# Performance work log

Measured on AMD Instinct MI355X. Metric: run time of the kernel, lower is better.

## Reference

```python
import math
import jax, jax.numpy as jnp
import numpy as np

NUM_HEADS = 8
NUM_LANDMARKS = 64
MP_ITERS = 6


def moore_penrose_iter_pinv(x, iters=MP_ITERS):
    # x: [..., m, m]; iterative Newton-Schulz-style pseudo-inverse
    abs_x = jnp.abs(x)
    col = abs_x.sum(axis=-1)
    row = abs_x.sum(axis=-2)
    z = jnp.swapaxes(x, -1, -2) / (jnp.max(col) * jnp.max(row))
    I = jnp.eye(x.shape[-1], dtype=x.dtype)
    for _ in range(iters):
        xz = x @ z
        z = 0.25 * z @ (13.0 * I - xz @ (15.0 * I - xz @ (7.0 * I - xz)))
    return z


def setup_inputs() -> dict:
    key = jax.random.key(0)
    k_x, k_qkv, k_proj = jax.random.split(key, 3)
    B, T, E = 2, 2048, 512
    x = jax.random.normal(k_x, (B, T, E), dtype=jnp.float32)
    w_qkv = jax.random.normal(k_qkv, (E, 3 * E), dtype=jnp.float32) * 0.02
    b_qkv = jnp.zeros((3 * E,), dtype=jnp.float32)
    w_proj = jax.random.normal(k_proj, (E, E), dtype=jnp.float32) * 0.02
    b_proj = jnp.zeros((E,), dtype=jnp.float32)
    return {"x": x, "w_qkv": w_qkv, "b_qkv": b_qkv, "w_proj": w_proj, "b_proj": b_proj}


def reference(x, w_qkv, b_qkv, w_proj, b_proj):
    B, T, E = x.shape
    H = NUM_HEADS
    M = NUM_LANDMARKS
    hd = E // H
    # T chosen as a multiple of M so the original pad branch is a no-op
    qkv = x @ w_qkv + b_qkv  # [B,T,3E]
    q, k, v = jnp.split(qkv, 3, axis=-1)

    def to_heads(t):
        return t.reshape(B, T, H, hd).transpose(0, 2, 1, 3)  # [B,H,T,hd]

    q = to_heads(q) * (1.0 / math.sqrt(hd))
    k = to_heads(k)
    v = to_heads(v)

    l = T // M  # landmark group size
    q_landmarks = q.reshape(B, H, M, l, hd).mean(axis=3)  # [B,H,M,hd]
    k_landmarks = k.reshape(B, H, M, l, hd).mean(axis=3)  # [B,H,M,hd]

    q_kl = jnp.einsum('bhid,bhjd->bhij', q, k_landmarks)           # [B,H,T,M]
    ql_kl = jnp.einsum('bhid,bhjd->bhij', q_landmarks, k_landmarks)  # [B,H,M,M]
    ql_k = jnp.einsum('bhid,bhjd->bhij', q_landmarks, k)           # [B,H,M,T]

    neg_inf = float('-inf')
    mask_q_kl = jnp.tril(jnp.ones((T, M), dtype=bool))
    mask_ql_kl = jnp.tril(jnp.ones((M, M), dtype=bool))
    mask_ql_k = jnp.tril(jnp.ones((M, T), dtype=bool))

    F_t = jax.nn.softmax(jnp.where(mask_q_kl, q_kl, neg_inf), axis=-1)    # [B,H,T,M]
    A = jax.nn.softmax(jnp.where(mask_ql_kl, ql_kl, neg_inf), axis=-1)    # [B,H,M,M]
    B_t = jax.nn.softmax(jnp.where(mask_ql_k, ql_k, neg_inf), axis=-1)    # [B,H,M,T]

    A_t = moore_penrose_iter_pinv(A, iters=MP_ITERS)

    attn = (F_t @ A_t) @ B_t  # [B,H,T,T] (original materializes this for dropout)
    y = attn @ v              # [B,H,T,hd]
    y = y.transpose(0, 2, 1, 3).reshape(B, T, E)
    return y @ w_proj + b_proj
```

## Files before the change

kernel.cpp:

```cpp
#include <hip/hip_runtime.h>
#include <hip/hip_bf16.h>

#define TB 2048
#define EB 512

using short8 = __attribute__((ext_vector_type(8))) short;
using f32x4  = __attribute__((ext_vector_type(4))) float;

__global__ __launch_bounds__(256) void k_pool(const float* __restrict__ x,
                                              float* __restrict__ xp,
                                              unsigned int* __restrict__ scal_u) {
  if (blockIdx.x == 0 && threadIdx.x == 0) scal_u[0] = 0u;
  int idx = blockIdx.x * 256 + threadIdx.x;
  int b = idx >> 15;
  int rem = idx & 32767;
  int m = rem >> 9;
  int e = rem & 511;
  const float* src = x + (b * TB + m * 32) * EB + e;
  float s = 0.f;
#pragma unroll
  for (int i = 0; i < 32; ++i) s += src[i * EB];
  xp[idx] = s * (1.f / 32.f);
}

__device__ __forceinline__ int swz_idx(int row, int col) {
  return row * 64 + ((((col >> 3) ^ (row & 7)) << 3) | (col & 7));
}

__device__ __forceinline__ void split_bf(float v, ushort& h, ushort& l) {
  __hip_bfloat16 bh = __float2bfloat16(v);
  float fh = __bfloat162float(bh);
  __hip_bfloat16 bl = __float2bfloat16(v - fh);
  h = *(ushort*)&bh;
  l = *(ushort*)&bl;
}

__device__ __forceinline__ void mm_frags(const short8 ah[2], const short8 al[2],
                                         const ushort* bhp, const ushort* blp,
                                         int lane, f32x4 acc[4]) {
  const int g = lane >> 4, li = lane & 15;
#pragma unroll
  for (int nt = 0; nt < 4; ++nt) {
    f32x4 a = acc[nt];
#pragma unroll
    for (int kh = 0; kh < 2; ++kh) {
      int n = nt * 16 + li;
      int k0 = kh * 32 + 8 * g;
      int idx = n * 64 + ((((k0 >> 3) ^ (n & 7)) << 3));
      short8 bh = *(const short8*)&bhp[idx];
      short8 bl = *(const short8*)&blp[idx];
      a = __builtin_amdgcn_mfma_f32_16x16x32_bf16(al[kh], bh, a, 0, 0, 0);
      a = __builtin_amdgcn_mfma_f32_16x16x32_bf16(ah[kh], bl, a, 0, 0, 0);
      a = __builtin_amdgcn_mfma_f32_16x16x32_bf16(ah[kh], bh, a, 0, 0, 0);
    }
    acc[nt] = a;
  }
}

__device__ __forceinline__ void zero_acc(f32x4 acc[4]) {
#pragma unroll
  for (int nt = 0; nt < 4; ++nt) acc[nt] = (f32x4){0.f, 0.f, 0.f, 0.f};
}

__device__ __forceinline__ void softmax_rows(f32x4 s[4], int band, int g, int li,
                                             bool causal, int t0) {
#pragma unroll
  for (int r = 0; r < 4; ++r) {
    int trow = t0 + band + 4 * g + r;
    float m = -1e30f;
    float sv[4];
#pragma unroll
    for (int nt = 0; nt < 4; ++nt) {
      int col = nt * 16 + li;
      bool ok = !causal || (col <= trow);
      sv[nt] = ok ? s[nt][r] : -1e30f;
      m = fmaxf(m, sv[nt]);
    }
    m = fmaxf(m, __shfl_xor(m, 1));
    m = fmaxf(m, __shfl_xor(m, 2));
    m = fmaxf(m, __shfl_xor(m, 4));
    m = fmaxf(m, __shfl_xor(m, 8));
    float su = 0.f;
    float ee[4];
#pragma unroll
    for (int nt = 0; nt < 4; ++nt) {
      ee[nt] = (sv[nt] > -1e29f) ? __expf(sv[nt] - m) : 0.f;
      su += ee[nt];
    }
    su += __shfl_xor(su, 1);
    su += __shfl_xor(su, 2);
    su += __shfl_xor(su, 4);
    su += __shfl_xor(su, 8);
    float inv = 1.f / su;
#pragma unroll
    for (int nt = 0; nt < 4; ++nt) s[nt][r] = ee[nt] * inv;
  }
}

__device__ __forceinline__ void wrP(ushort* hp, ushort* lp, int lane,
                                    const f32x4 acc[4]) {
  const int g = lane >> 4, li = lane & 15;
#pragma unroll
  for (int nt = 0; nt < 4; ++nt) {
    int c = nt * 16 + li;
#pragma unroll
    for (int r = 0; r < 4; ++r) {
      int row = 4 * g + r;
      ushort h, l;
      split_bf(acc[nt][r], h, l);
      int idx = swz_idx(row, c);
      hp[idx] = h;
      lp[idx] = l;
    }
  }
}

__device__ __forceinline__ void ld_pfrags(const ushort* hp, const ushort* lp,
                                          int lane, short8 ah[2], short8 al[2]) {
  const int g = lane >> 4, li = lane & 15;
#pragma unroll
  for (int kh = 0; kh < 2; ++kh) {
    int k0 = kh * 32 + 8 * g;
    int idx = li * 64 + ((((k0 >> 3) ^ (li & 7)) << 3));
    ah[kh] = *(const short8*)&hp[idx];
    al[kh] = *(const short8*)&lp[idx];
  }
}

template <int MODE>
__global__ __launch_bounds__(256) void k_gemm_mfma(const float* __restrict__ A,
                                                   const float* __restrict__ A2,
                                                   const float* __restrict__ W,
                                                   const float* __restrict__ bias,
                                                   float* __restrict__ o0,
                                                   float* __restrict__ o1,
                                                   float* __restrict__ o2,
                                                   float* __restrict__ o3) {
  constexpr int LDW = (MODE == 1) ? 512 : 1536;
  __shared__ ushort Ah[4096], Al[4096], Bh[4096], Bl[4096];
  const int tid = threadIdx.x;
  const int lane = tid & 63, w = tid >> 6, band = w * 16;
  int bx, by;
  if constexpr (MODE == 0 || MODE == 1) {
    int bid = blockIdx.x;
    by = ((bid & 7) << 3) | (bid >> 6);
    bx = (bid >> 3) & 7;
  } else {
    bx = blockIdx.x;
    by = blockIdx.y;
  }
  const int variant = (MODE == 2) ? (by >> 1) : 0;
  const int m0 = (MODE == 2) ? ((by & 1) * 64) : by * 64;
  const int bcol0 = (MODE == 2) ? (variant == 0 ? 512 + bx * 64 : bx * 64)
                                : bx * 64;
  const int g = lane >> 4, li = lane & 15;

  const int arow = tid >> 2, akc = (tid & 3) * 16;
  const int bn = tid & 63, bkc = (tid >> 6) * 16;

  const float* asrc;
  {
    int gr = m0 + arow;
    if constexpr (MODE == 2) {
      asrc = (variant == 0) ? (A + ((gr >> 6) * TB + (gr & 63)) * EB)
                            : (A2 + gr * EB);
    } else {
      asrc = A + gr * EB;
    }
  }

  f32x4 acc[4];
  zero_acc(acc);

  float av[16], bv[16];
#pragma unroll
  for (int j = 0; j < 4; ++j)
    *(float4*)&av[j * 4] = *(const float4*)&asrc[akc + j * 4];
#pragma unroll
  for (int i = 0; i < 16; ++i) bv[i] = W[(bkc + i) * LDW + bcol0 + bn];

#pragma unroll
  for (int k0 = 0; k0 < 512; k0 += 64) {
    if (k0) __syncthreads();
#pragma unroll
    for (int c2 = 0; c2 < 2; ++c2) {
      short8 hv, lv;
#pragma unroll
      for (int i = 0; i < 8; ++i) {
        ushort h, l;
        split_bf(av[c2 * 8 + i], h, l);
        hv[i] = (short)h;
        lv[i] = (short)l;
      }
      int chunk = ((akc >> 3) + c2) ^ (arow & 7);
      int idx = arow * 64 + chunk * 8;
      *(short8*)&Ah[idx] = hv;
      *(short8*)&Al[idx] = lv;
    }
#pragma unroll
    for (int c2 = 0; c2 < 2; ++c2) {
      short8 hv, lv;
#pragma unroll
      for (int i = 0; i < 8; ++i) {
        ushort h, l;
        split_bf(bv[c2 * 8 + i], h, l);
        hv[i] = (short)h;
        lv[i] = (short)l;
      }
      int chunk = ((bkc >> 3) + c2) ^ (bn & 7);
      int idx = bn * 64 + chunk * 8;
      *(short8*)&Bh[idx] = hv;
      *(short8*)&Bl[idx] = lv;
    }
    __syncthreads();
    if (k0 + 64 < 512) {
#pragma unroll
      for (int j = 0; j < 4; ++j)
        *(float4*)&av[j * 4] = *(const float4*)&asrc[k0 + 64 + akc + j * 4];
#pragma unroll
      for (int i = 0; i < 16; ++i)
        bv[i] = W[(k0 + 64 + bkc + i) * LDW + bcol0 + bn];
    }
    short8 a_h[2], a_l[2];
    const int row = band + li;
#pragma unroll
    for (int kh = 0; kh < 2; ++kh) {
      int chunk = ((kh * 32 + 8 * g) >> 3) ^ (row & 7);
      int idx = row * 64 + chunk * 8;
      a_h[kh] = *(const short8*)&Ah[idx];
      a_l[kh] = *(const short8*)&Al[idx];
    }
    mm_frags(a_h, a_l, Bh, Bl, lane, acc);
  }
#pragma unroll
  for (int nt = 0; nt < 4; ++nt) {
#pragma unroll
    for (int r = 0; r < 4; ++r) {
      int trow = band + 4 * g + r;
      int gcol = bcol0 + nt * 16 + li;
      float v = acc[nt][r] + bias[gcol];
      if constexpr (MODE == 1) {
        o0[(m0 + trow) * 512 + gcol] = v;
      } else {
        int gr = m0 + trow;
        int b = gr >> 6, t = gr & 63;
        int cloc = (variant == 0) ? (gcol - 512) : gcol;
        int which = cloc >> 9;
        int hd_ = cloc & 511;
        int h = hd_ >> 6, d = hd_ & 63;
        int dst = ((b * 8 + h) * 64 + t) * 64 + d;
        if (variant == 0) {
          if (which == 0) o0[dst] = v; else o1[dst] = v;
        } else {
          if (which == 0) o2[dst] = v * 0.125f; else o3[dst] = v;
        }
      }
    }
  }
}

__global__ __launch_bounds__(256) void k_abv_w2(
    const float* __restrict__ qlg, const float* __restrict__ klg,
    const float* __restrict__ k64, const float* __restrict__ v64,
    const float* __restrict__ w_qkv, const float* __restrict__ b_qkv,
    float* __restrict__ A, float* __restrict__ BV,
    float* __restrict__ W2g, float* __restrict__ bcst,
    unsigned int* __restrict__ scal_u) {
  __shared__ ushort KLh[4096], KLl[4096], Kh[4096], Kl_[4096], VTh[4096], VTl[4096];
  __shared__ ushort Ph[4][1024], Pl[4][1024];
  __shared__ float red[4][64];
  const int tid = threadIdx.x;
  const int lane = tid & 63, w = tid >> 6, band = w * 16;
  const int g = lane >> 4, li = lane & 15;

  if (blockIdx.x >= 16) {
    const int bh = blockIdx.x - 16;
    const int h = bh & 7;
    const int base = bh * 4096;
    {
      int n = tid & 63, kc = (tid >> 6) * 16;
      float a[16];
#pragma unroll
      for (int i = 0; i < 16; ++i) a[i] = klg[base + n * 64 + kc + i];
#pragma unroll
      for (int c2 = 0; c2 < 2; ++c2) {
        int idx = n * 64 + ((((kc >> 3) + c2) ^ (n & 7)) << 3);
        short8 hv, lv;
#pragma unroll
        for (int i = 0; i < 8; ++i) {
          ushort hh, ll;
          split_bf(a[c2 * 8 + i], hh, ll);
          hv[i] = (short)hh;
          lv[i] = (short)ll;
        }
        *(short8*)&KLh[idx] = hv;
        *(short8*)&KLl[idx] = lv;
      }
    }
    __syncthreads();
    if (tid < 64) {
      float bc = 0.f;
      for (int d = 0; d < 64; ++d)
        bc += b_qkv[h * 64 + d] * klg[base + tid * 64 + d];
      bcst[bh * 64 + tid] = 0.125f * bc;
    }
#pragma unroll
    for (int m0 = 0; m0 < 512; m0 += 64) {
      short8 a_h[2], a_l[2];
      int row = m0 + band + li;
#pragma unroll
      for (int kh = 0; kh < 2; ++kh) {
        int d0 = kh * 32 + 8 * g;
        float tmp[8];
        *(float4*)&tmp[0] = *(const float4*)&w_qkv[row * 1536 + h * 64 + d0];
        *(float4*)&tmp[4] = *(const float4*)&w_qkv[row * 1536 + h * 64 + d0 + 4];
        short8 hv, lv;
#pragma unroll
        for (int i = 0; i < 8; ++i) {
          ushort hh, ll;
          split_bf(tmp[i], hh, ll);
          hv[i] = (short)hh;
          lv[i] = (short)ll;
        }
        a_h[kh] = hv;
        a_l[kh] = lv;
      }
      f32x4 acc[4];
      zero_acc(acc);
      mm_frags(a_h, a_l, KLh, KLl, lane, acc);
#pragma unroll
      for (int nt = 0; nt < 4; ++nt)
#pragma unroll
        for (int r = 0; r < 4; ++r)
          W2g[bh * 32768 + (m0 + band + 4 * g + r) * 64 + nt * 16 + li] =
              0.125f * acc[nt][r];
    }
    return;
  }

  const int bh = blockIdx.x;
  const int base = bh * 4096;
  {
    int n = tid & 63, kc = (tid >> 6) * 16;
    float a[16], b[16], c[16];
#pragma unroll
    for (int i = 0; i < 16; ++i) {
      a[i] = klg[base + n * 64 + kc + i];
      b[i] = k64[base + n * 64 + kc + i];
      c[i] = v64[base + (kc + i) * 64 + n];
    }
#pragma unroll
    for (int c2 = 0; c2 < 2; ++c2) {
      int idx = n * 64 + ((((kc >> 3) + c2) ^ (n & 7)) << 3);
      short8 hv, lv;
#pragma unroll
      for (int i = 0; i < 8; ++i) { ushort h, l; split_bf(a[c2*8+i], h, l); hv[i]=(short)h; lv[i]=(short)l; }
      *(short8*)&KLh[idx] = hv; *(short8*)&KLl[idx] = lv;
#pragma unroll
      for (int i = 0; i < 8; ++i) { ushort h, l; split_bf(b[c2*8+i], h, l); hv[i]=(short)h; lv[i]=(short)l; }
      *(short8*)&Kh[idx] = hv; *(short8*)&Kl_[idx] = lv;
#pragma unroll
      for (int i = 0; i < 8; ++i) { ushort h, l; split_bf(c[c2*8+i], h, l); hv[i]=(short)h; lv[i]=(short)l; }
      *(short8*)&VTh[idx] = hv; *(short8*)&VTl[idx] = lv;
    }
  }
  short8 q_h[2], q_l[2];
  {
    int row = band + li;
#pragma unroll
    for (int kh = 0; kh < 2; ++kh) {
      int k0 = kh * 32 + 8 * g;
      float tmp[8];
      *(float4*)&tmp[0] = *(const float4*)&qlg[base + row * 64 + k0];
      *(float4*)&tmp[4] = *(const float4*)&qlg[base + row * 64 + k0 + 4];
      short8 hv, lv;
#pragma unroll
      for (int i = 0; i < 8; ++i) { ushort h, l; split_bf(tmp[i], h, l); hv[i]=(short)h; lv[i]=(short)l; }
      q_h[kh] = hv; q_l[kh] = lv;
    }
  }
  __syncthreads();
  f32x4 s1[4];
  zero_acc(s1);
  mm_frags(q_h, q_l, KLh, KLl, lane, s1);
  softmax_rows(s1, band, g, li, true, 0);
#pragma unroll
  for (int nt = 0; nt < 4; ++nt)
#pragma unroll
    for (int r = 0; r < 4; ++r)
      A[base + (band + 4 * g + r) * 64 + nt * 16 + li] = s1[nt][r];
  {
    float part[4];
#pragma unroll
    for (int nt = 0; nt < 4; ++nt) {
      part[nt] = s1[nt][0] + s1[nt][1] + s1[nt][2] + s1[nt][3];
      part[nt] += __shfl_xor(part[nt], 16);
      part[nt] += __shfl_xor(part[nt], 32);
    }
    if (g == 0) {
#pragma unroll
      for (int nt = 0; nt < 4; ++nt) red[w][nt * 16 + li] = part[nt];
    }
    __syncthreads();
    if (tid < 64) {
      float t = red[0][tid] + red[1][tid] + red[2][tid] + red[3][tid];
#pragma unroll
      for (int off = 32; off; off >>= 1) t = fmaxf(t, __shfl_xor(t, off));
      if (tid == 0) atomicMax(scal_u, __float_as_uint(t));
    }
  }
  f32x4 s2[4];
  zero_acc(s2);
  mm_frags(q_h, q_l, Kh, Kl_, lane, s2);
  softmax_rows(s2, band, g, li, true, 0);
  wrP(Ph[w], Pl[w], lane, s2);
  short8 p_h[2], p_l[2];
  ld_pfrags(Ph[w], Pl[w], lane, p_h, p_l);
  f32x4 y[4];
  zero_acc(y);
  mm_frags(p_h, p_l, VTh, VTl, lane, y);
#pragma unroll
  for (int nt = 0; nt < 4; ++nt)
#pragma unroll
    for (int r = 0; r < 4; ++r)
      BV[base + (band + 4 * g + r) * 64 + nt * 16 + li] = y[nt][r];
}

__device__ __forceinline__ void ld_afrags(const ushort* hp, const ushort* lp,
                                          int band, int lane,
                                          short8 ah[2], short8 al[2]) {
  const int g = lane >> 4, li = lane & 15;
  const int row = band + li;
#pragma unroll
  for (int kh = 0; kh < 2; ++kh) {
    int k0 = kh * 32 + 8 * g;
    int idx = row * 64 + ((((k0 >> 3) ^ (row & 7)) << 3));
    ah[kh] = *(const short8*)&hp[idx];
    al[kh] = *(const short8*)&lp[idx];
  }
}

__device__ __forceinline__ void mm_frags0(const short8 ah[2], const short8 al[2],
                                          const ushort* bhp, const ushort* blp,
                                          int lane, f32x4 acc[4]) {
  zero_acc(acc);
  mm_frags(ah, al, bhp, blp, lane, acc);
}

__device__ __forceinline__ void wrT(ushort* hp, ushort* lp, int band, int lane,
                                    const f32x4 acc[4], float cI, float mul) {
  const int g = lane >> 4, li = lane & 15;
  const int r0 = band + 4 * g;
#pragma unroll
  for (int nt = 0; nt < 4; ++nt) {
    int c = nt * 16 + li;
    ushort h[4], l[4];
#pragma unroll
    for (int r = 0; r < 4; ++r) {
      float v = mul * acc[nt][r] + ((r0 + r) == c ? cI : 0.f);
      split_bf(v, h[r], l[r]);
    }
    int idx = c * 64 + (((((r0) >> 3) ^ (c & 7)) << 3) | (r0 & 7));
    *(ushort4*)&hp[idx] = make_ushort4(h[0], h[1], h[2], h[3]);
    *(ushort4*)&lp[idx] = make_ushort4(l[0], l[1], l[2], l[3]);
  }
}

__device__ __forceinline__ void wrN(ushort* hp, ushort* lp, int band, int lane,
                                    const f32x4 acc[4], float mul) {
  const int g = lane >> 4, li = lane & 15;
#pragma unroll
  for (int nt = 0; nt < 4; ++nt) {
    int c = nt * 16 + li;
#pragma unroll
    for (int r = 0; r < 4; ++r) {
      int row = band + 4 * g + r;
      ushort h, l;
      split_bf(mul * acc[nt][r], h, l);
      int idx = swz_idx(row, c);
      hp[idx] = h;
      lp[idx] = l;
    }
  }
}

__global__ __launch_bounds__(256) void k_pinv(const float* __restrict__ A,
                                              const float* __restrict__ BVg,
                                              const unsigned int* __restrict__ scal_u,
                                              float* __restrict__ C) {
  __shared__ ushort ZT_h[4096], ZT_l[4096], ZA_h[4096], ZA_l[4096],
                    PA_h[4096], PA_l[4096], QA_h[4096], QA_l[4096],
                    QB_h[4096], QB_l[4096], BT_h[4096], BT_l[4096];
  const int bh = blockIdx.x, tid = threadIdx.x;
  const int lane = tid & 63, w = tid >> 6, band = w * 16;
  const int base = bh * 4096;
  const float sc = 1.f / __uint_as_float(scal_u[0]);
  const float* Ag = A + base;
  const float* Bg = BVg + base;

  {
    int prow = tid >> 2;
    int pc0 = (tid & 3) * 16;
#pragma unroll 4
    for (int j = 0; j < 16; ++j) {
      int col = pc0 + j;
      float av = Ag[prow * 64 + col] * sc;
      ushort h, l;
      split_bf(av, h, l);
      int i1 = swz_idx(prow, col);
      ZT_h[i1] = h; ZT_l[i1] = l;
      int i2 = swz_idx(col, prow);
      ZA_h[i2] = h; ZA_l[i2] = l;
      float bv = Bg[prow * 64 + col];
      split_bf(bv, h, l);
      BT_h[i2] = h; BT_l[i2] = l;
    }
  }
  short8 a_h[2], a_l[2];
  {
    const int g = lane >> 4, li = lane & 15;
    int row = band + li;
#pragma unroll
    for (int kh = 0; kh < 2; ++kh) {
      int k0 = kh * 32 + 8 * g;
      float tmp[8];
      *(float4*)&tmp[0] = *(const float4*)&Ag[row * 64 + k0];
      *(float4*)&tmp[4] = *(const float4*)&Ag[row * 64 + k0 + 4];
      short8 hv, lv;
#pragma unroll
      for (int i = 0; i < 8; ++i) {
        ushort h, l;
        split_bf(tmp[i], h, l);
        hv[i] = (short)h;
        lv[i] = (short)l;
      }
      a_h[kh] = hv;
      a_l[kh] = lv;
    }
  }
  __syncthreads();

  for (int it = 0; it < 6; ++it) {
    f32x4 acc[4];
    mm_frags0(a_h, a_l, ZT_h, ZT_l, lane, acc);
    wrN(PA_h, PA_l, band, lane, acc, 1.f);
    wrT(QA_h, QA_l, band, lane, acc, 7.f, -1.f);
    __syncthreads();
    short8 p_h[2], p_l[2];
    ld_afrags(PA_h, PA_l, band, lane, p_h, p_l);
    mm_frags0(p_h, p_l, QA_h, QA_l, lane, acc);
    wrT(QB_h, QB_l, band, lane, acc, 15.f, -1.f);
    __syncthreads();
    mm_frags0(p_h, p_l, QB_h, QB_l, lane, acc);
    wrT(QA_h, QA_l, band, lane, acc, 13.f, -1.f);
    __syncthreads();
    short8 z_h[2], z_l[2];
    ld_afrags(ZA_h, ZA_l, band, lane, z_h, z_l);
    mm_frags0(z_h, z_l, QA_h, QA_l, lane, acc);
    wrN(ZA_h, ZA_l, band, lane, acc, 0.25f);
    wrT(ZT_h, ZT_l, band, lane, acc, 0.f, 0.25f);
    __syncthreads();
  }
  {
    short8 z_h[2], z_l[2];
    ld_afrags(ZA_h, ZA_l, band, lane, z_h, z_l);
    f32x4 acc[4];
    mm_frags0(z_h, z_l, BT_h, BT_l, lane, acc);
    const int g = lane >> 4, li = lane & 15;
#pragma unroll
    for (int nt = 0; nt < 4; ++nt) {
#pragma unroll
      for (int r = 0; r < 4; ++r) {
        int row = band + 4 * g + r;
        int col = nt * 16 + li;
        C[base + row * 64 + col] = acc[nt][r];
      }
    }
  }
}

__global__ __launch_bounds__(256) void k_f_y2(const float* __restrict__ x,
                                              const float* __restrict__ W2g,
                                              const float* __restrict__ bcst,
                                              const float* __restrict__ C,
                                              float* __restrict__ yh) {
  __shared__ ushort Ah[4096], Al[4096], Bh[4096], Bl[4096];
  __shared__ ushort CTh[4096], CTl[4096];
  __shared__ ushort Ph[4][1024], Pl[4][1024];
  const int tid = threadIdx.x;
  const int lane = tid & 63, w = tid >> 6, band = w * 16;
  const int bid = blockIdx.x;
  const int by = ((bid & 7) << 3) | (bid >> 6);
  const int bx = (bid >> 3) & 7;
  const int b = by >> 5, t0 = (by & 31) * 64, h = bx;
  const int bh = b * 8 + h;
  const int g = lane >> 4, li = lane & 15;
  const int arow = tid >> 2, akc = (tid & 3) * 16;
  const int bn = tid & 63, bkc = (tid >> 6) * 16;
  const float* asrc = x + (b * TB + t0 + arow) * EB;
  const float* wsrc = W2g + bh * 32768;
  const int base = bh * 4096;

  {
    int n = tid & 63, kc = (tid >> 6) * 16;
    float c[16];
#pragma unroll
    for (int i = 0; i < 16; ++i) c[i] = C[base + (kc + i) * 64 + n];
#pragma unroll
    for (int c2 = 0; c2 < 2; ++c2) {
      int idx = n * 64 + ((((kc >> 3) + c2) ^ (n & 7)) << 3);
      short8 hv, lv;
#pragma unroll
      for (int i = 0; i < 8; ++i) {
        ushort hh, ll;
        split_bf(c[c2 * 8 + i], hh, ll);
        hv[i] = (short)hh;
        lv[i] = (short)ll;
      }
      *(short8*)&CTh[idx] = hv;
      *(short8*)&CTl[idx] = lv;
    }
  }

  f32x4 acc[4];
  zero_acc(acc);
  float av[16], bv[16];
#pragma unroll
  for (int j = 0; j < 4; ++j)
    *(float4*)&av[j * 4] = *(const float4*)&asrc[akc + j * 4];
#pragma unroll
  for (int i = 0; i < 16; ++i) bv[i] = wsrc[(bkc + i) * 64 + bn];

#pragma unroll
  for (int k0 = 0; k0 < 512; k0 += 64) {
    if (k0) __syncthreads();
#pragma unroll
    for (int c2 = 0; c2 < 2; ++c2) {
      short8 hv, lv;
#pragma unroll
      for (int i = 0; i < 8; ++i) {
        ushort hh, ll;
        split_bf(av[c2 * 8 + i], hh, ll);
        hv[i] = (short)hh;
        lv[i] = (short)ll;
      }
      int chunk = ((akc >> 3) + c2) ^ (arow & 7);
      int idx = arow * 64 + chunk * 8;
      *(short8*)&Ah[idx] = hv;
      *(short8*)&Al[idx] = lv;
    }
#pragma unroll
    for (int c2 = 0; c2 < 2; ++c2) {
      short8 hv, lv;
#pragma unroll
      for (int i = 0; i < 8; ++i) {
        ushort hh, ll;
        split_bf(bv[c2 * 8 + i], hh, ll);
        hv[i] = (short)hh;
        lv[i] = (short)ll;
      }
      int chunk = ((bkc >> 3) + c2) ^ (bn & 7);
      int idx = bn * 64 + chunk * 8;
      *(short8*)&Bh[idx] = hv;
      *(short8*)&Bl[idx] = lv;
    }
    __syncthreads();
    if (k0 + 64 < 512) {
#pragma unroll
      for (int j = 0; j < 4; ++j)
        *(float4*)&av[j * 4] = *(const float4*)&asrc[k0 + 64 + akc + j * 4];
#pragma unroll
      for (int i = 0; i < 16; ++i)
        bv[i] = wsrc[(k0 + 64 + bkc + i) * 64 + bn];
    }
    short8 a_h[2], a_l[2];
    const int row = band + li;
#pragma unroll
    for (int kh = 0; kh < 2; ++kh) {
      int chunk = ((kh * 32 + 8 * g) >> 3) ^ (row & 7);
      int idx = row * 64 + chunk * 8;
      a_h[kh] = *(const short8*)&Ah[idx];
      a_l[kh] = *(const short8*)&Al[idx];
    }
    mm_frags(a_h, a_l, Bh, Bl, lane, acc);
  }
#pragma unroll
  for (int nt = 0; nt < 4; ++nt) {
    float bc = bcst[bh * 64 + nt * 16 + li];
#pragma unroll
    for (int r = 0; r < 4; ++r) acc[nt][r] += bc;
  }
  softmax_rows(acc, band, g, li, t0 == 0, 0);
  wrP(Ph[w], Pl[w], lane, acc);
  short8 p_h[2], p_l[2];
  ld_pfrags(Ph[w], Pl[w], lane, p_h, p_l);
  f32x4 y[4];
  zero_acc(y);
  mm_frags(p_h, p_l, CTh, CTl, lane, y);
#pragma unroll
  for (int nt = 0; nt < 4; ++nt)
#pragma unroll
    for (int r = 0; r < 4; ++r) {
      int t = t0 + band + 4 * g + r;
      int d = nt * 16 + li;
      yh[(b * 2048 + t) * 512 + h * 64 + d] = y[nt][r];
    }
}

extern "C" void kernel_launch(void* const* d_in, const int* in_sizes, int n_in,
                              void* d_out, int out_size, void* d_ws, size_t ws_size,
                              hipStream_t stream) {
  const float* x = (const float*)d_in[0];
  const float* w_qkv = (const float*)d_in[1];
  const float* b_qkv = (const float*)d_in[2];
  const float* w_proj = (const float*)d_in[3];
  const float* b_proj = (const float*)d_in[4];
  float* out = (float*)d_out;

  float* ws = (float*)d_ws;
  float* W2 = ws;
  float* bcst = ws + 524288;
  float* k64 = ws + 2097152;
  float* v64 = k64 + 65536;
  float* xp = v64 + 65536;
  float* ql = xp + 65536;
  float* kl = ql + 65536;
  float* Am = kl + 65536;
  float* BV = Am + 65536;
  float* Cm = BV + 65536;
  unsigned int* scal_u = (unsigned int*)(Cm + 65536);
  float* yh = (float*)(scal_u + 64);

  k_pool<<<dim3(256), dim3(256), 0, stream>>>(x, xp, scal_u);
  k_gemm_mfma<2><<<dim3(16, 4), dim3(256), 0, stream>>>(x, xp, w_qkv, b_qkv,
                                                        k64, v64, ql, kl);
  k_abv_w2<<<dim3(32), dim3(256), 0, stream>>>(ql, kl, k64, v64, w_qkv, b_qkv,
                                               Am, BV, W2, bcst, scal_u);
  k_pinv<<<dim3(16), dim3(256), 0, stream>>>(Am, BV, scal_u, Cm);
  k_f_y2<<<dim3(512), dim3(256), 0, stream>>>(x, W2, bcst, Cm, yh);
  k_gemm_mfma<1><<<dim3(512), dim3(256), 0, stream>>>(yh, nullptr, w_proj, b_proj,
                                                      out, nullptr, nullptr, nullptr);
}
```

Measured before the change: 139.3 us.

## Fuse pinv into landmark kernel and store presplit bf16 operands for downstream GEMMs

Merges the A/BV computation with the Moore-Penrose pseudo-inverse into one kernel, removing a launch and the global atomic max, since each block now computes its own scale locally. W2, the C matrix, the attention output and w_proj are now written as pre-split, swizzled bf16 hi/lo tiles, so later kernels can load them straight into shared memory without re-splitting. The projection GEMM becomes a dedicated kernel with double-buffered register prefetch of the pre-split weights. Risks: the pinv scale is now computed per (batch, head) block instead of globally, which could change numerics; it also uses more shared memory per block in the fused kernel.

```diff
diff --git a/kernel.cpp b/kernel.cpp
--- a/kernel.cpp
+++ b/kernel.cpp
@@ -6,22 +6,6 @@
 
 using short8 = __attribute__((ext_vector_type(8))) short;
 using f32x4  = __attribute__((ext_vector_type(4))) float;
-
-__global__ __launch_bounds__(256) void k_pool(const float* __restrict__ x,
-                                              float* __restrict__ xp,
-                                              unsigned int* __restrict__ scal_u) {
-  if (blockIdx.x == 0 && threadIdx.x == 0) scal_u[0] = 0u;
-  int idx = blockIdx.x * 256 + threadIdx.x;
-  int b = idx >> 15;
-  int rem = idx & 32767;
-  int m = rem >> 9;
-  int e = rem & 511;
-  const float* src = x + (b * TB + m * 32) * EB + e;
-  float s = 0.f;
-#pragma unroll
-  for (int i = 0; i < 32; ++i) s += src[i * EB];
-  xp[idx] = s * (1.f / 32.f);
-}
 
 __device__ __forceinline__ int swz_idx(int row, int col) {
   return row * 64 + ((((col >> 3) ^ (row & 7)) << 3) | (col & 7));
@@ -127,51 +111,127 @@
   }
 }
 
-template <int MODE>
-__global__ __launch_bounds__(256) void k_gemm_mfma(const float* __restrict__ A,
-                                                   const float* __restrict__ A2,
-                                                   const float* __restrict__ W,
-                                                   const float* __restrict__ bias,
-                                                   float* __restrict__ o0,
-                                                   float* __restrict__ o1,
-                                                   float* __restrict__ o2,
-                                                   float* __restrict__ o3) {
-  constexpr int LDW = (MODE == 1) ? 512 : 1536;
+__device__ __forceinline__ void ld_afrags(const ushort* hp, const ushort* lp,
+                                          int band, int lane,
+                                          short8 ah[2], short8 al[2]) {
+  const int g = lane >> 4, li = lane & 15;
+  const int row = band + li;
+#pragma unroll
+  for (int kh = 0; kh < 2; ++kh) {
+    int k0 = kh * 32 + 8 * g;
+    int idx = row * 64 + ((((k0 >> 3) ^ (row & 7)) << 3));
+    ah[kh] = *(const short8*)&hp[idx];
+    al[kh] = *(const short8*)&lp[idx];
+  }
+}
+
+__device__ __forceinline__ void mm_frags0(const short8 ah[2], const short8 al[2],
+                                          const ushort* bhp, const ushort* blp,
+                                          int lane, f32x4 acc[4]) {
+  zero_acc(acc);
+  mm_frags(ah, al, bhp, blp, lane, acc);
+}
+
+__device__ __forceinline__ void wrT(ushort* hp, ushort* lp, int band, int lane,
+                                    const f32x4 acc[4], float cI, float mul) {
+  const int g = lane >> 4, li = lane & 15;
+  const int r0 = band + 4 * g;
+#pragma unroll
+  for (int nt = 0; nt < 4; ++nt) {
+    int c = nt * 16 + li;
+    ushort h[4], l[4];
+#pragma unroll
+    for (int r = 0; r < 4; ++r) {
+      float v = mul * acc[nt][r] + ((r0 + r) == c ? cI : 0.f);
+      split_bf(v, h[r], l[r]);
+    }
+    int idx = c * 64 + (((((r0) >> 3) ^ (c & 7)) << 3) | (r0 & 7));
+    *(ushort4*)&hp[idx] = make_ushort4(h[0], h[1], h[2], h[3]);
+    *(ushort4*)&lp[idx] = make_ushort4(l[0], l[1], l[2], l[3]);
+  }
+}
+
+__device__ __forceinline__ void wrN(ushort* hp, ushort* lp, int band, int lane,
+                                    const f32x4 acc[4], float mul) {
+  const int g = lane >> 4, li = lane & 15;
+#pragma unroll
+  for (int nt = 0; nt < 4; ++nt) {
+    int c = nt * 16 + li;
+#pragma unroll
+    for (int r = 0; r < 4; ++r) {
+      int row = band + 4 * g + r;
+      ushort h, l;
+      split_bf(mul * acc[nt][r], h, l);
+      int idx = swz_idx(row, c);
+      hp[idx] = h;
+      lp[idx] = l;
+    }
+  }
+}
+
+__global__ __launch_bounds__(256) void k_pool(const float* __restrict__ x,
+                                              const float* __restrict__ w_proj,
+                                              float* __restrict__ xp,
+                                              ushort* __restrict__ WpH,
+                                              ushort* __restrict__ WpL) {
+  const int tid = threadIdx.x;
+  if (blockIdx.x >= 256) {
+    int t = blockIdx.x - 256;
+    int bxp = t >> 3, kt = t & 7;
+    int n = tid & 63, kc = (tid >> 6) * 16;
+#pragma unroll
+    for (int i = 0; i < 16; ++i) {
+      int k = kc + i;
+      float v = w_proj[(kt * 64 + k) * 512 + bxp * 64 + n];
+      ushort h, l;
+      split_bf(v, h, l);
+      int idx = t * 4096 + swz_idx(n, k);
+      WpH[idx] = h;
+      WpL[idx] = l;
+    }
+    return;
+  }
+  int idx = blockIdx.x * 256 + tid;
+  int b = idx >> 15;
+  int rem = idx & 32767;
+  int m = rem >> 9;
+  int e = rem & 511;
+  const float* src = x + (b * TB + m * 32) * EB + e;
+  float s = 0.f;
+#pragma unroll
+  for (int i = 0; i < 32; ++i) s += src[i * EB];
+  xp[idx] = s * (1.f / 32.f);
+}
+
+__global__ __launch_bounds__(256) void k_small(const float* __restrict__ A,
+                                               const float* __restrict__ A2,
+                                               const float* __restrict__ W,
+                                               const float* __restrict__ bias,
+                                               float* __restrict__ o0,
+                                               float* __restrict__ o1,
+                                               float* __restrict__ o2,
+                                               float* __restrict__ o3) {
+  constexpr int LDW = 1536;
   __shared__ ushort Ah[4096], Al[4096], Bh[4096], Bl[4096];
   const int tid = threadIdx.x;
   const int lane = tid & 63, w = tid >> 6, band = w * 16;
-  int bx, by;
-  if constexpr (MODE == 0 || MODE == 1) {
-    int bid = blockIdx.x;
-    by = ((bid & 7) << 3) | (bid >> 6);
-    bx = (bid >> 3) & 7;
-  } else {
-    bx = blockIdx.x;
-    by = blockIdx.y;
-  }
-  const int variant = (MODE == 2) ? (by >> 1) : 0;
-  const int m0 = (MODE == 2) ? ((by & 1) * 64) : by * 64;
-  const int bcol0 = (MODE == 2) ? (variant == 0 ? 512 + bx * 64 : bx * 64)
-                                : bx * 64;
-  const int g = lane >> 4, li = lane & 15;
-
+  const int bx = blockIdx.x, by = blockIdx.y;
+  const int variant = by >> 1;
+  const int m0 = (by & 1) * 64;
+  const int bcol0 = (variant == 0 ? 512 + bx * 64 : bx * 64);
+  const int g = lane >> 4, li = lane & 15;
   const int arow = tid >> 2, akc = (tid & 3) * 16;
   const int bn = tid & 63, bkc = (tid >> 6) * 16;
 
   const float* asrc;
   {
     int gr = m0 + arow;
-    if constexpr (MODE == 2) {
-      asrc = (variant == 0) ? (A + ((gr >> 6) * TB + (gr & 63)) * EB)
-                            : (A2 + gr * EB);
-    } else {
-      asrc = A + gr * EB;
-    }
+    asrc = (variant == 0) ? (A + ((gr >> 6) * TB + (gr & 63)) * EB)
+                          : (A2 + gr * EB);
   }
 
   f32x4 acc[4];
   zero_acc(acc);
-
   float av[16], bv[16];
 #pragma unroll
   for (int j = 0; j < 4; ++j)
@@ -239,36 +299,32 @@
       int trow = band + 4 * g + r;
       int gcol = bcol0 + nt * 16 + li;
       float v = acc[nt][r] + bias[gcol];
-      if constexpr (MODE == 1) {
-        o0[(m0 + trow) * 512 + gcol] = v;
+      int gr = m0 + trow;
+      int b = gr >> 6, t = gr & 63;
+      int cloc = (variant == 0) ? (gcol - 512) : gcol;
+      int which = cloc >> 9;
+      int hd_ = cloc & 511;
+      int h = hd_ >> 6, d = hd_ & 63;
+      int dst = ((b * 8 + h) * 64 + t) * 64 + d;
+      if (variant == 0) {
+        if (which == 0) o0[dst] = v; else o1[dst] = v;
       } else {
-        int gr = m0 + trow;
-        int b = gr >> 6, t = gr & 63;
-        int cloc = (variant == 0) ? (gcol - 512) : gcol;
-        int which = cloc >> 9;
-        int hd_ = cloc & 511;
-        int h = hd_ >> 6, d = hd_ & 63;
-        int dst = ((b * 8 + h) * 64 + t) * 64 + d;
-        if (variant == 0) {
-          if (which == 0) o0[dst] = v; else o1[dst] = v;
-        } else {
-          if (which == 0) o2[dst] = v * 0.125f; else o3[dst] = v;
-        }
+        if (which == 0) o2[dst] = v * 0.125f; else o3[dst] = v;
       }
     }
   }
 }
 
-__global__ __launch_bounds__(256) void k_abv_w2(
+__global__ __launch_bounds__(256) void k_abv_pinv(
     const float* __restrict__ qlg, const float* __restrict__ klg,
     const float* __restrict__ k64, const float* __restrict__ v64,
     const float* __restrict__ w_qkv, const float* __restrict__ b_qkv,
-    float* __restrict__ A, float* __restrict__ BV,
-    float* __restrict__ W2g, float* __restrict__ bcst,
-    unsigned int* __restrict__ scal_u) {
-  __shared__ ushort KLh[4096], KLl[4096], Kh[4096], Kl_[4096], VTh[4096], VTl[4096];
-  __shared__ ushort Ph[4][1024], Pl[4][1024];
+    ushort* __restrict__ W2H, ushort* __restrict__ W2L,
+    float* __restrict__ bcst,
+    ushort* __restrict__ CTH, ushort* __restrict__ CTL) {
+  __shared__ ushort pl[12][4096];
   __shared__ float red[4][64];
+  __shared__ float scs;
   const int tid = threadIdx.x;
   const int lane = tid & 63, w = tid >> 6, band = w * 16;
   const int g = lane >> 4, li = lane & 15;
@@ -293,8 +349,8 @@
           hv[i] = (short)hh;
           lv[i] = (short)ll;
         }
-        *(short8*)&KLh[idx] = hv;
-        *(short8*)&KLl[idx] = lv;
+        *(short8*)&pl[0][idx] = hv;
+        *(short8*)&pl[1][idx] = lv;
       }
     }
     __syncthreads();
@@ -326,14 +382,9 @@
         a_l[kh] = lv;
       }
       f32x4 acc[4];
-      zero_acc(acc);
-      mm_frags(a_h, a_l, KLh, KLl, lane, acc);
-#pragma unroll
-      for (int nt = 0; nt < 4; ++nt)
-#pragma unroll
-        for (int r = 0; r < 4; ++r)
-          W2g[bh * 32768 + (m0 + band + 4 * g + r) * 64 + nt * 16 + li] =
-              0.125f * acc[nt][r];
+      mm_frags0(a_h, a_l, pl[0], pl[1], lane, acc);
+      wrT(W2H + bh * 32768 + (m0 >> 6) * 4096,
+          W2L + bh * 32768 + (m0 >> 6) * 4096, band, lane, acc, 0.f, 0.125f);
     }
     return;
   }
@@ -355,13 +406,13 @@
       short8 hv, lv;
 #pragma unroll
       for (int i = 0; i < 8; ++i) { ushort h, l; split_bf(a[c2*8+i], h, l); hv[i]=(short)h; lv[i]=(short)l; }
-      *(short8*)&KLh[idx] = hv; *(short8*)&KLl[idx] = lv;
+      *(short8*)&pl[0][idx] = hv; *(short8*)&pl[1][idx] = lv;
 #pragma unroll
       for (int i = 0; i < 8; ++i) { ushort h, l; split_bf(b[c2*8+i], h, l); hv[i]=(short)h; lv[i]=(short)l; }
-      *(short8*)&Kh[idx] = hv; *(short8*)&Kl_[idx] = lv;
+      *(short8*)&pl[2][idx] = hv; *(short8*)&pl[3][idx] = lv;
 #pragma unroll
       for (int i = 0; i < 8; ++i) { ushort h, l; split_bf(c[c2*8+i], h, l); hv[i]=(short)h; lv[i]=(short)l; }
-      *(short8*)&VTh[idx] = hv; *(short8*)&VTl[idx] = lv;
+      *(short8*)&pl[4][idx] = hv; *(short8*)&pl[5][idx] = lv;
     }
   }
   short8 q_h[2], q_l[2];
@@ -381,14 +432,8 @@
   }
   __syncthreads();
   f32x4 s1[4];
-  zero_acc(s1);
-  mm_frags(q_h, q_l, KLh, KLl, lane, s1);
+  mm_frags0(q_h, q_l, pl[0], pl[1], lane, s1);
   softmax_rows(s1, band, g, li, true, 0);
-#pragma unroll
-  for (int nt = 0; nt < 4; ++nt)
-#pragma unroll
-    for (int r = 0; r < 4; ++r)
-      A[base + (band + 4 * g + r) * 64 + nt * 16 + li] = s1[nt][r];
   {
     float part[4];
 #pragma unroll
@@ -406,187 +451,68 @@
       float t = red[0][tid] + red[1][tid] + red[2][tid] + red[3][tid];
 #pragma unroll
       for (int off = 32; off; off >>= 1) t = fmaxf(t, __shfl_xor(t, off));
-      if (tid == 0) atomicMax(scal_u, __float_as_uint(t));
-    }
-  }
+      if (tid == 0) scs = 1.f / t;
+    }
+    __syncthreads();
+  }
+  const float sc = scs;
   f32x4 s2[4];
-  zero_acc(s2);
-  mm_frags(q_h, q_l, Kh, Kl_, lane, s2);
+  mm_frags0(q_h, q_l, pl[2], pl[3], lane, s2);
   softmax_rows(s2, band, g, li, true, 0);
-  wrP(Ph[w], Pl[w], lane, s2);
+  wrP(&pl[6][w * 1024], &pl[7][w * 1024], lane, s2);
   short8 p_h[2], p_l[2];
-  ld_pfrags(Ph[w], Pl[w], lane, p_h, p_l);
+  ld_pfrags(&pl[6][w * 1024], &pl[7][w * 1024], lane, p_h, p_l);
   f32x4 y[4];
-  zero_acc(y);
-  mm_frags(p_h, p_l, VTh, VTl, lane, y);
-#pragma unroll
-  for (int nt = 0; nt < 4; ++nt)
-#pragma unroll
-    for (int r = 0; r < 4; ++r)
-      BV[base + (band + 4 * g + r) * 64 + nt * 16 + li] = y[nt][r];
-}
-
-__device__ __forceinline__ void ld_afrags(const ushort* hp, const ushort* lp,
-                                          int band, int lane,
-                                          short8 ah[2], short8 al[2]) {
-  const int g = lane >> 4, li = lane & 15;
-  const int row = band + li;
-#pragma unroll
-  for (int kh = 0; kh < 2; ++kh) {
-    int k0 = kh * 32 + 8 * g;
-    int idx = row * 64 + ((((k0 >> 3) ^ (row & 7)) << 3));
-    ah[kh] = *(const short8*)&hp[idx];
-    al[kh] = *(const short8*)&lp[idx];
-  }
-}
-
-__device__ __forceinline__ void mm_frags0(const short8 ah[2], const short8 al[2],
-                                          const ushort* bhp, const ushort* blp,
-                                          int lane, f32x4 acc[4]) {
-  zero_acc(acc);
-  mm_frags(ah, al, bhp, blp, lane, acc);
-}
-
-__device__ __forceinline__ void wrT(ushort* hp, ushort* lp, int band, int lane,
-                                    const f32x4 acc[4], float cI, float mul) {
-  const int g = lane >> 4, li = lane & 15;
-  const int r0 = band + 4 * g;
-#pragma unroll
-  for (int nt = 0; nt < 4; ++nt) {
-    int c = nt * 16 + li;
-    ushort h[4], l[4];
-#pragma unroll
-    for (int r = 0; r < 4; ++r) {
-      float v = mul * acc[nt][r] + ((r0 + r) == c ? cI : 0.f);
-      split_bf(v, h[r], l[r]);
-    }
-    int idx = c * 64 + (((((r0) >> 3) ^ (c & 7)) << 3) | (r0 & 7));
-    *(ushort4*)&hp[idx] = make_ushort4(h[0], h[1], h[2], h[3]);
-    *(ushort4*)&lp[idx] = make_ushort4(l[0], l[1], l[2], l[3]);
-  }
-}
-
-__device__ __forceinline__ void wrN(ushort* hp, ushort* lp, int band, int lane,
-                                    const f32x4 acc[4], float mul) {
-  const int g = lane >> 4, li = lane & 15;
-#pragma unroll
-  for (int nt = 0; nt < 4; ++nt) {
-    int c = nt * 16 + li;
-#pragma unroll
-    for (int r = 0; r < 4; ++r) {
-      int row = band + 4 * g + r;
-      ushort h, l;
-      split_bf(mul * acc[nt][r], h, l);
-      int idx = swz_idx(row, c);
-      hp[idx] = h;
-      lp[idx] = l;
-    }
-  }
-}
-
-__global__ __launch_bounds__(256) void k_pinv(const float* __restrict__ A,
-                                              const float* __restrict__ BVg,
-                                              const unsigned int* __restrict__ scal_u,
-                                              float* __restrict__ C) {
-  __shared__ ushort ZT_h[4096], ZT_l[4096], ZA_h[4096], ZA_l[4096],
-                    PA_h[4096], PA_l[4096], QA_h[4096], QA_l[4096],
-                    QB_h[4096], QB_l[4096], BT_h[4096], BT_l[4096];
-  const int bh = blockIdx.x, tid = threadIdx.x;
-  const int lane = tid & 63, w = tid >> 6, band = w * 16;
-  const int base = bh * 4096;
-  const float sc = 1.f / __uint_as_float(scal_u[0]);
-  const float* Ag = A + base;
-  const float* Bg = BVg + base;
-
-  {
-    int prow = tid >> 2;
-    int pc0 = (tid & 3) * 16;
-#pragma unroll 4
-    for (int j = 0; j < 16; ++j) {
-      int col = pc0 + j;
-      float av = Ag[prow * 64 + col] * sc;
-      ushort h, l;
-      split_bf(av, h, l);
-      int i1 = swz_idx(prow, col);
-      ZT_h[i1] = h; ZT_l[i1] = l;
-      int i2 = swz_idx(col, prow);
-      ZA_h[i2] = h; ZA_l[i2] = l;
-      float bv = Bg[prow * 64 + col];
-      split_bf(bv, h, l);
-      BT_h[i2] = h; BT_l[i2] = l;
-    }
-  }
+  mm_frags0(p_h, p_l, pl[4], pl[5], lane, y);
+  __syncthreads();
+  wrT(pl[8], pl[9], band, lane, y, 0.f, 1.f);
+  wrN(pl[10], pl[11], band, lane, s1, sc);
+  wrT(pl[2], pl[3], band, lane, s1, 0.f, sc);
+  wrN(pl[0], pl[1], band, lane, s1, 1.f);
+  __syncthreads();
   short8 a_h[2], a_l[2];
-  {
-    const int g = lane >> 4, li = lane & 15;
-    int row = band + li;
-#pragma unroll
-    for (int kh = 0; kh < 2; ++kh) {
-      int k0 = kh * 32 + 8 * g;
-      float tmp[8];
-      *(float4*)&tmp[0] = *(const float4*)&Ag[row * 64 + k0];
-      *(float4*)&tmp[4] = *(const float4*)&Ag[row * 64 + k0 + 4];
-      short8 hv, lv;
-#pragma unroll
-      for (int i = 0; i < 8; ++i) {
-        ushort h, l;
-        split_bf(tmp[i], h, l);
-        hv[i] = (short)h;
-        lv[i] = (short)l;
-      }
-      a_h[kh] = hv;
-      a_l[kh] = lv;
-    }
-  }
+  ld_afrags(pl[0], pl[1], band, lane, a_h, a_l);
   __syncthreads();
-
   for (int it = 0; it < 6; ++it) {
     f32x4 acc[4];
-    mm_frags0(a_h, a_l, ZT_h, ZT_l, lane, acc);
-    wrN(PA_h, PA_l, band, lane, acc, 1.f);
-    wrT(QA_h, QA_l, band, lane, acc, 7.f, -1.f);
-    __syncthreads();
-    short8 p_h[2], p_l[2];
-    ld_afrags(PA_h, PA_l, band, lane, p_h, p_l);
-    mm_frags0(p_h, p_l, QA_h, QA_l, lane, acc);
-    wrT(QB_h, QB_l, band, lane, acc, 15.f, -1.f);
-    __syncthreads();
-    mm_frags0(p_h, p_l, QB_h, QB_l, lane, acc);
-    wrT(QA_h, QA_l, band, lane, acc, 13.f, -1.f);
+    mm_frags0(a_h, a_l, pl[10], pl[11], lane, acc);
+    wrN(pl[4], pl[5], band, lane, acc, 1.f);
+    wrT(pl[6], pl[7], band, lane, acc, 7.f, -1.f);
+    __syncthreads();
+    short8 pp_h[2], pp_l[2];
+    ld_afrags(pl[4], pl[5], band, lane, pp_h, pp_l);
+    mm_frags0(pp_h, pp_l, pl[6], pl[7], lane, acc);
+    wrT(pl[0], pl[1], band, lane, acc, 15.f, -1.f);
+    __syncthreads();
+    mm_frags0(pp_h, pp_l, pl[0], pl[1], lane, acc);
+    wrT(pl[6], pl[7], band, lane, acc, 13.f, -1.f);
     __syncthreads();
     short8 z_h[2], z_l[2];
-    ld_afrags(ZA_h, ZA_l, band, lane, z_h, z_l);
-    mm_frags0(z_h, z_l, QA_h, QA_l, lane, acc);
-    wrN(ZA_h, ZA_l, band, lane, acc, 0.25f);
-    wrT(ZT_h, ZT_l, band, lane, acc, 0.f, 0.25f);
+    ld_afrags(pl[2], pl[3], band, lane, z_h, z_l);
+    mm_frags0(z_h, z_l, pl[6], pl[7], lane, acc);
+    __syncthreads();
+    wrN(pl[2], pl[3], band, lane, acc, 0.25f);
+    wrT(pl[10], pl[11], band, lane, acc, 0.f, 0.25f);
     __syncthreads();
   }
   {
     short8 z_h[2], z_l[2];
-    ld_afrags(ZA_h, ZA_l, band, lane, z_h, z_l);
+    ld_afrags(pl[2], pl[3], band, lane, z_h, z_l);
     f32x4 acc[4];
-    mm_frags0(z_h, z_l, BT_h, BT_l, lane, acc);
-    const int g = lane >> 4, li = lane & 15;
-#pragma unroll
-    for (int nt = 0; nt < 4; ++nt) {
-#pragma unroll
-      for (int r = 0; r < 4; ++r) {
-        int row = band + 4 * g + r;
-        int col = nt * 16 + li;
-        C[base + row * 64 + col] = acc[nt][r];
-      }
-    }
+    mm_frags0(z_h, z_l, pl[8], pl[9], lane, acc);
+    wrT(CTH + bh * 4096, CTL + bh * 4096, band, lane, acc, 0.f, 1.f);
   }
 }
 
 __global__ __launch_bounds__(256) void k_f_y2(const float* __restrict__ x,
-                                              const float* __restrict__ W2g,
+                                              const ushort* __restrict__ W2H,
+                                              const ushort* __restrict__ W2L,
                                               const float* __restrict__ bcst,
-                                              const float* __restrict__ C,
-                                              float* __restrict__ yh) {
-  __shared__ ushort Ah[4096], Al[4096], Bh[4096], Bl[4096];
-  __shared__ ushort CTh[4096], CTl[4096];
-  __shared__ ushort Ph[4][1024], Pl[4][1024];
+                                              const ushort* __restrict__ CTH,
+                                              const ushort* __restrict__ CTL,
+                                              ushort* __restrict__ yhH,
+                                              ushort* __restrict__ yhL) {
+  __shared__ ushort Bh[4096], Bl[4096], CTs_h[4096], CTs_l[4096];
   const int tid = threadIdx.x;
   const int lane = tid & 63, w = tid >> 6, band = w * 16;
   const int bid = blockIdx.x;
@@ -595,116 +521,162 @@
   const int b = by >> 5, t0 = (by & 31) * 64, h = bx;
   const int bh = b * 8 + h;
   const int g = lane >> 4, li = lane & 15;
-  const int arow = tid >> 2, akc = (tid & 3) * 16;
-  const int bn = tid & 63, bkc = (tid >> 6) * 16;
-  const float* asrc = x + (b * TB + t0 + arow) * EB;
-  const float* wsrc = W2g + bh * 32768;
-  const int base = bh * 4096;
 
   {
-    int n = tid & 63, kc = (tid >> 6) * 16;
-    float c[16];
-#pragma unroll
-    for (int i = 0; i < 16; ++i) c[i] = C[base + (kc + i) * 64 + n];
-#pragma unroll
-    for (int c2 = 0; c2 < 2; ++c2) {
-      int idx = n * 64 + ((((kc >> 3) + c2) ^ (n & 7)) << 3);
+    const ushort* sh = CTH + bh * 4096;
+    const ushort* sl = CTL + bh * 4096;
+    *(short8*)&CTs_h[tid * 8] = *(const short8*)&sh[tid * 8];
+    *(short8*)&CTs_h[2048 + tid * 8] = *(const short8*)&sh[2048 + tid * 8];
+    *(short8*)&CTs_l[tid * 8] = *(const short8*)&sl[tid * 8];
+    *(short8*)&CTs_l[2048 + tid * 8] = *(const short8*)&sl[2048 + tid * 8];
+  }
+  const ushort* wH = W2H + bh * 32768;
+  const ushort* wL = W2L + bh * 32768;
+  const float* xrow = x + (b * TB + t0 + band + li) * EB;
+
+  f32x4 acc[4];
+  zero_acc(acc);
+  float a8[2][2][8];
+  short8 rb[2][4];
+#pragma unroll
+  for (int kh = 0; kh < 2; ++kh) {
+    *(float4*)&a8[0][kh][0] = *(const float4*)&xrow[kh * 32 + 8 * g];
+    *(float4*)&a8[0][kh][4] = *(const float4*)&xrow[kh * 32 + 8 * g + 4];
+  }
+  rb[0][0] = *(const short8*)&wH[tid * 8];
+  rb[0][1] = *(const short8*)&wH[2048 + tid * 8];
+  rb[0][2] = *(const short8*)&wL[tid * 8];
+  rb[0][3] = *(const short8*)&wL[2048 + tid * 8];
+
+#pragma unroll
+  for (int kt = 0; kt < 8; ++kt) {
+    const int cur = kt & 1, nxt = cur ^ 1;
+    if (kt) __syncthreads();
+    *(short8*)&Bh[tid * 8] = rb[cur][0];
+    *(short8*)&Bh[2048 + tid * 8] = rb[cur][1];
+    *(short8*)&Bl[tid * 8] = rb[cur][2];
+    *(short8*)&Bl[2048 + tid * 8] = rb[cur][3];
+    __syncthreads();
+    if (kt < 7) {
+      int k0 = (kt + 1) * 64;
+#pragma unroll
+      for (int kh = 0; kh < 2; ++kh) {
+        *(float4*)&a8[nxt][kh][0] = *(const float4*)&xrow[k0 + kh * 32 + 8 * g];
+        *(float4*)&a8[nxt][kh][4] = *(const float4*)&xrow[k0 + kh * 32 + 8 * g + 4];
+      }
+      const ushort* wHt = wH + (kt + 1) * 4096;
+      const ushort* wLt = wL + (kt + 1) * 4096;
+      rb[nxt][0] = *(const short8*)&wHt[tid * 8];
+      rb[nxt][1] = *(const short8*)&wHt[2048 + tid * 8];
+      rb[nxt][2] = *(const short8*)&wLt[tid * 8];
+      rb[nxt][3] = *(const short8*)&wLt[2048 + tid * 8];
+    }
+    short8 a_h[2], a_l[2];
+#pragma unroll
+    for (int kh = 0; kh < 2; ++kh) {
       short8 hv, lv;
 #pragma unroll
       for (int i = 0; i < 8; ++i) {
         ushort hh, ll;
-        split_bf(c[c2 * 8 + i], hh, ll);
+        split_bf(a8[cur][kh][i], hh, ll);
         hv[i] = (short)hh;
         lv[i] = (short)ll;
       }
-      *(short8*)&CTh[idx] = hv;
-      *(short8*)&CTl[idx] = lv;
-    }
-  }
+      a_h[kh] = hv;
+      a_l[kh] = lv;
+    }
+    mm_frags(a_h, a_l, Bh, Bl, lane, acc);
+  }
+#pragma unroll
+  for (int nt = 0; nt < 4; ++nt) {
+    float bc = bcst[bh * 64 + nt * 16 + li];
+#pragma unroll
+    for (int r = 0; r < 4; ++r) acc[nt][r] += bc;
+  }
+  softmax_rows(acc, band, g, li, t0 == 0, 0);
+  __syncthreads();
+  wrP(&Bh[w * 1024], &Bl[w * 1024], lane, acc);
+  short8 p_h[2], p_l[2];
+  ld_pfrags(&Bh[w * 1024], &Bl[w * 1024], lane, p_h, p_l);
+  f32x4 y[4];
+  mm_frags0(p_h, p_l, CTs_h, CTs_l, lane, y);
+  const int pb = (by * 8 + h) * 4096;
+#pragma unroll
+  for (int nt = 0; nt < 4; ++nt) {
+#pragma unroll
+    for (int r = 0; r < 4; ++r) {
+      ushort hh, ll;
+      split_bf(y[nt][r], hh, ll);
+      int idx = pb + swz_idx(band + 4 * g + r, nt * 16 + li);
+      yhH[idx] = hh;
+      yhL[idx] = ll;
+    }
+  }
+}
+
+__global__ __launch_bounds__(256) void k_proj(const ushort* __restrict__ yhH,
+                                              const ushort* __restrict__ yhL,
+                                              const ushort* __restrict__ WpH,
+                                              const ushort* __restrict__ WpL,
+                                              const float* __restrict__ bias,
+                                              float* __restrict__ out) {
+  __shared__ ushort Bh[4096], Bl[4096];
+  const int tid = threadIdx.x;
+  const int lane = tid & 63, w = tid >> 6, band = w * 16;
+  const int bid = blockIdx.x;
+  const int by = ((bid & 7) << 3) | (bid >> 6);
+  const int bx = (bid >> 3) & 7;
+  const int g = lane >> 4, li = lane & 15;
+  const ushort* aH = yhH + by * 32768;
+  const ushort* aL = yhL + by * 32768;
+  const ushort* wH = WpH + bx * 32768;
+  const ushort* wL = WpL + bx * 32768;
 
   f32x4 acc[4];
   zero_acc(acc);
-  float av[16], bv[16];
-#pragma unroll
-  for (int j = 0; j < 4; ++j)
-    *(float4*)&av[j * 4] = *(const float4*)&asrc[akc + j * 4];
-#pragma unroll
-  for (int i = 0; i < 16; ++i) bv[i] = wsrc[(bkc + i) * 64 + bn];
-
-#pragma unroll
-  for (int k0 = 0; k0 < 512; k0 += 64) {
-    if (k0) __syncthreads();
-#pragma unroll
-    for (int c2 = 0; c2 < 2; ++c2) {
-      short8 hv, lv;
-#pragma unroll
-      for (int i = 0; i < 8; ++i) {
-        ushort hh, ll;
-        split_bf(av[c2 * 8 + i], hh, ll);
-        hv[i] = (short)hh;
-        lv[i] = (short)ll;
-      }
-      int chunk = ((akc >> 3) + c2) ^ (arow & 7);
-      int idx = arow * 64 + chunk * 8;
-      *(short8*)&Ah[idx] = hv;
-      *(short8*)&Al[idx] = lv;
-    }
-#pragma unroll
-    for (int c2 = 0; c2 < 2; ++c2) {
-      short8 hv, lv;
-#pragma unroll
-      for (int i = 0; i < 8; ++i) {
-        ushort hh, ll;
-        split_bf(bv[c2 * 8 + i], hh, ll);
-        hv[i] = (short)hh;
-        lv[i] = (short)ll;
-      }
-      int chunk = ((bkc >> 3) + c2) ^ (bn & 7);
-      int idx = bn * 64 + chunk * 8;
-      *(short8*)&Bh[idx] = hv;
-      *(short8*)&Bl[idx] = lv;
-    }
-    __syncthreads();
-    if (k0 + 64 < 512) {
-#pragma unroll
-      for (int j = 0; j < 4; ++j)
-        *(float4*)&av[j * 4] = *(const float4*)&asrc[k0 + 64 + akc + j * 4];
-#pragma unroll
-      for (int i = 0; i < 16; ++i)
-        bv[i] = wsrc[(k0 + 64 + bkc + i) * 64 + bn];
+  short8 rb[2][4];
+  rb[0][0] = *(const short8*)&wH[tid * 8];
+  rb[0][1] = *(const short8*)&wH[2048 + tid * 8];
+  rb[0][2] = *(const short8*)&wL[tid * 8];
+  rb[0][3] = *(const short8*)&wL[2048 + tid * 8];
+
+  const int row = band + li;
+#pragma unroll
+  for (int kt = 0; kt < 8; ++kt) {
+    const int cur = kt & 1, nxt = cur ^ 1;
+    if (kt) __syncthreads();
+    *(short8*)&Bh[tid * 8] = rb[cur][0];
+    *(short8*)&Bh[2048 + tid * 8] = rb[cur][1];
+    *(short8*)&Bl[tid * 8] = rb[cur][2];
+    *(short8*)&Bl[2048 + tid * 8] = rb[cur][3];
+    __syncthreads();
+    if (kt < 7) {
+      const ushort* wHt = wH + (kt + 1) * 4096;
+      const ushort* wLt = wL + (kt + 1) * 4096;
+      rb[nxt][0] = *(const short8*)&wHt[tid * 8];
+      rb[nxt][1] = *(const short8*)&wHt[2048 + tid * 8];
+      rb[nxt][2] = *(const short8*)&wLt[tid * 8];
+      rb[nxt][3] = *(const short8*)&wLt[2048 + tid * 8];
     }
     short8 a_h[2], a_l[2];
-    const int row = band + li;
 #pragma unroll
     for (int kh = 0; kh < 2; ++kh) {
       int chunk = ((kh * 32 + 8 * g) >> 3) ^ (row & 7);
-      int idx = row * 64 + chunk * 8;
-      a_h[kh] = *(const short8*)&Ah[idx];
-      a_l[kh] = *(const short8*)&Al[idx];
+      int idx = kt * 4096 + row * 64 + chunk * 8;
+      a_h[kh] = *(const short8*)&aH[idx];
+      a_l[kh] = *(const short8*)&aL[idx];
     }
     mm_frags(a_h, a_l, Bh, Bl, lane, acc);
   }
 #pragma unroll
   for (int nt = 0; nt < 4; ++nt) {
-    float bc = bcst[bh * 64 + nt * 16 + li];
-#pragma unroll
-    for (int r = 0; r < 4; ++r) acc[nt][r] += bc;
-  }
-  softmax_rows(acc, band, g, li, t0 == 0, 0);
-  wrP(Ph[w], Pl[w], lane, acc);
-  short8 p_h[2], p_l[2];
-  ld_pfrags(Ph[w], Pl[w], lane, p_h, p_l);
-  f32x4 y[4];
-  zero_acc(y);
-  mm_frags(p_h, p_l, CTh, CTl, lane, y);
-#pragma unroll
-  for (int nt = 0; nt < 4; ++nt)
 #pragma unroll
     for (int r = 0; r < 4; ++r) {
-      int t = t0 + band + 4 * g + r;
-      int d = nt * 16 + li;
-      yh[(b * 2048 + t) * 512 + h * 64 + d] = y[nt][r];
-    }
+      int trow = by * 64 + band + 4 * g + r;
+      int gcol = bx * 64 + nt * 16 + li;
+      out[trow * 512 + gcol] = acc[nt][r] + bias[gcol];
+    }
+  }
 }
 
 extern "C" void kernel_launch(void* const* d_in, const int* in_sizes, int n_in,
@@ -717,27 +689,28 @@
   const float* b_proj = (const float*)d_in[4];
   float* out = (float*)d_out;
 
-  float* ws = (float*)d_ws;
-  float* W2 = ws;
-  float* bcst = ws + 524288;
-  float* k64 = ws + 2097152;
-  float* v64 = k64 + 65536;
-  float* xp = v64 + 65536;
-  float* ql = xp + 65536;
-  float* kl = ql + 65536;
-  float* Am = kl + 65536;
-  float* BV = Am + 65536;
-  float* Cm = BV + 65536;
-  unsigned int* scal_u = (unsigned int*)(Cm + 65536);
-  float* yh = (float*)(scal_u + 64);
-
-  k_pool<<<dim3(256), dim3(256), 0, stream>>>(x, xp, scal_u);
-  k_gemm_mfma<2><<<dim3(16, 4), dim3(256), 0, stream>>>(x, xp, w_qkv, b_qkv,
-                                                        k64, v64, ql, kl);
-  k_abv_w2<<<dim3(32), dim3(256), 0, stream>>>(ql, kl, k64, v64, w_qkv, b_qkv,
-                                               Am, BV, W2, bcst, scal_u);
-  k_pinv<<<dim3(16), dim3(256), 0, stream>>>(Am, BV, scal_u, Cm);
-  k_f_y2<<<dim3(512), dim3(256), 0, stream>>>(x, W2, bcst, Cm, yh);
-  k_gemm_mfma<1><<<dim3(512), dim3(256), 0, stream>>>(yh, nullptr, w_proj, b_proj,
-                                                      out, nullptr, nullptr, nullptr);
-}
+  char* base = (char*)d_ws;
+  ushort* W2H = (ushort*)(base);
+  ushort* W2L = (ushort*)(base + (1 << 20));
+  float* bcst = (float*)(base + (2 << 20));
+  ushort* CTH = (ushort*)(base + (2 << 20) + (1 << 16));
+  ushort* CTL = (ushort*)(base + (2 << 20) + (3 << 16));
+  ushort* WpH = (ushort*)(base + (3 << 20));
+  ushort* WpL = (ushort*)(base + (3 << 20) + (1 << 19));
+  ushort* yhH = (ushort*)(base + (4 << 20));
+  ushort* yhL = (ushort*)(base + (8 << 20));
+  float* k64 = (float*)(base + (12 << 20));
+  float* v64 = (float*)(base + (13 << 20));
+  float* xp  = (float*)(base + (14 << 20));
+  float* ql  = (float*)(base + (15 << 20));
+  float* kl  = (float*)(base + (16 << 20));
+
+  k_pool<<<dim3(320), dim3(256), 0, stream>>>(x, w_proj, xp, WpH, WpL);
+  k_small<<<dim3(16, 4), dim3(256), 0, stream>>>(x, xp, w_qkv, b_qkv,
+                                                 k64, v64, ql, kl);
+  k_abv_pinv<<<dim3(32), dim3(256), 0, stream>>>(ql, kl, k64, v64, w_qkv, b_qkv,
+                                                 W2H, W2L, bcst, CTH, CTL);
+  k_f_y2<<<dim3(512), dim3(256), 0, stream>>>(x, W2H, W2L, bcst, CTH, CTL,
+                                              yhH, yhL);
+  k_proj<<<dim3(512), dim3(256), 0, stream>>>(yhH, yhL, WpH, WpL, b_proj, out);
+}
```

New measurement: 135.6 us. 2.7% less time.
